# Performance work log

Hardware: AMD Instinct MI355X
Metric: run time of the kernel (lower is better)

The kernel has to match this reference:

```python
import jax, jax.numpy as jnp
import numpy as np

NEG = -1e30  # log-domain "zero" (safe in fp32/bf16 logaddexp)
EPS = 1e-7   # keras backend epsilon used by K.ctc_batch_cost


def setup_inputs() -> dict:
    key = jax.random.key(0)
    k1, k2 = jax.random.split(key)
    B, T, C, L = 64, 1024, 512, 128
    y_pred = jax.random.uniform(k1, (B, T, C), dtype=jnp.float32)
    y_true = jax.random.randint(k2, (B, L), 0, C - 1)  # blank = C-1 excluded
    return {"y_true": y_true, "y_pred": y_pred}


def ctc_batch_cost(y_true, y_pred):
    """Faithful jax port of keras.backend.ctc_batch_cost with full-length
    labels/inputs (as the CTCLayer passes input_length=T, label_length=L
    for every batch element). Returns per-example loss of shape [B, 1].

    K.ctc_batch_cost computes log(y_pred + eps) and feeds it to
    tf.nn.ctc_loss, which applies an internal softmax; we replicate that
    with log_softmax(log(y_pred + eps)). blank index = C - 1.
    """
    B, T, C = y_pred.shape
    L = y_true.shape[1]
    blank = C - 1
    logp = jax.nn.log_softmax(jnp.log(y_pred + EPS), axis=-1)  # [B,T,C]

    # Extended label sequence with interleaved blanks: length S = 2L+1
    S = 2 * L + 1
    ext = jnp.full((B, S), blank, dtype=y_true.dtype).at[:, 1::2].set(y_true)
    ext_m2 = jnp.concatenate(
        [jnp.full((B, 2), -1, dtype=ext.dtype), ext[:, :-2]], axis=1)
    # alpha[s-2] -> alpha[s] skip allowed iff ext[s] != blank and ext[s] != ext[s-2]
    skip = (ext != blank) & (ext != ext_m2)  # [B,S]

    # Emission log-probs gathered along the extended sequence: [B,T,S]
    emit = jnp.take_along_axis(
        logp, jnp.broadcast_to(ext[:, None, :], (B, T, S)), axis=2)

    # alpha_0: only states 0 (blank) and 1 (first label) are reachable
    alpha0 = (jnp.full((B, S), NEG, dtype=logp.dtype)
              .at[:, 0].set(emit[:, 0, 0])
              .at[:, 1].set(emit[:, 0, 1]))

    neg1 = jnp.full((B, 1), NEG, dtype=logp.dtype)
    neg2 = jnp.full((B, 2), NEG, dtype=logp.dtype)

    def step(alpha, emit_t):
        a1 = jnp.concatenate([neg1, alpha[:, :-1]], axis=1)   # stay->next
        a2 = jnp.concatenate([neg2, alpha[:, :-2]], axis=1)   # skip blank
        a2 = jnp.where(skip, a2, NEG)
        comb = jnp.logaddexp(jnp.logaddexp(alpha, a1), a2)
        return comb + emit_t, None

    emit_tm = jnp.transpose(emit, (1, 0, 2))  # time-major [T,B,S]
    alphaT, _ = jax.lax.scan(step, alpha0, emit_tm[1:])

    # p(labels) = alpha_T[S-1] + alpha_T[S-2]
    loss = -jnp.logaddexp(alphaT[:, -1], alphaT[:, -2])  # [B]
    return loss[:, None]


def reference(y_true, y_pred):
    return ctc_batch_cost(y_true, y_pred)
```

## Files before the change

kernel.cpp:

```cpp
#include <hip/hip_runtime.h>


#define EPSF 1e-7f
static constexpr int NB = 64;
static constexpr int NT = 1024;
static constexpr int NC = 512;
static constexpr int NL = 128;
static constexpr int CHUNK = 32;
static constexpr int NCH = NT / CHUNK;

typedef unsigned int uint32;
typedef float v2f __attribute__((ext_vector_type(2)));

__device__ __forceinline__ unsigned short rn_bf16(float x) {
    uint32 b = __float_as_uint(x);
    return (unsigned short)((b + 0x7FFFu + ((b >> 16) & 1u)) >> 16);
}

__global__ __launch_bounds__(256) void ctc_prep(const float* __restrict__ Y,
                                                const int* __restrict__ y_true,
                                                uint32* __restrict__ qlab,
                                                float* __restrict__ eblank,
                                                int mode) {
    const int lane = threadIdx.x & 63;
    const int wslot = threadIdx.x >> 6;
    const int nw = gridDim.x * 4;

    for (int w = blockIdx.x * 4 + wslot; w < NB * NT; w += nw) {
        int b = w >> 10;
        const float* row = Y + (size_t)w * NC;

        float4 v0 = *reinterpret_cast<const float4*>(row + lane * 4);
        float4 v1 = *reinterpret_cast<const float4*>(row + (NC / 2) + lane * 4);
        float s = ((v0.x + v0.y) + (v0.z + v0.w)) +
                  ((v1.x + v1.y) + (v1.z + v1.w));
#pragma unroll
        for (int d = 1; d < 64; d <<= 1) s += __shfl_xor(s, d);

        if (mode == 1) {
            float rb = row[NC - 1] + EPSF;
            float inv = 1.0f / (s + NC * EPSF);
            float rbi = 1.0f / rb;
            int2 lp = *reinterpret_cast<const int2*>(y_true + b * NL + lane * 2);
            float qx = (row[lp.x] + EPSF) * rbi;
            float qy = (row[lp.y] + EPSF) * rbi;
            uint32 pk = (uint32)rn_bf16(qx) | ((uint32)rn_bf16(qy) << 16);
            qlab[(size_t)w * (NL / 2) + lane] = pk;
            if (lane == 0) eblank[w] = rb * inv;
        } else {
            if (lane == 0) eblank[w] = 256.0f / (s + NC * EPSF);
        }
    }
}

__device__ __forceinline__ float dpp_wave_shr1(float x) {
    return __int_as_float(__builtin_amdgcn_update_dpp(
        0, __float_as_int(x), 0x138, 0xF, 0xF, true));
}

__device__ __forceinline__ float dpp_wave_max(float m) {
#define DPPMAX_(ctrl)                                                     \
    m = fmaxf(m, __int_as_float(__builtin_amdgcn_update_dpp(              \
                     0, __float_as_int(m), ctrl, 0xF, 0xF, true)))
    DPPMAX_(0x111); DPPMAX_(0x112); DPPMAX_(0x114); DPPMAX_(0x118);
    DPPMAX_(0x142); DPPMAX_(0x143);
#undef DPPMAX_
    return __int_as_float(
        __builtin_amdgcn_readlane(__float_as_int(m), 63));
}

__device__ __forceinline__ float dpp_wave_sum63(float v) {
#define DPPADD_(ctrl)                                                     \
    v += __int_as_float(__builtin_amdgcn_update_dpp(                      \
        0, __float_as_int(v), ctrl, 0xF, 0xF, true))
    DPPADD_(0x111); DPPADD_(0x112); DPPADD_(0x114); DPPADD_(0x118);
    DPPADD_(0x142); DPPADD_(0x143);
#undef DPPADD_
    return v;
}

__global__ __launch_bounds__(64) void ctc_rec1(const uint32* __restrict__ A,
                                               const float* __restrict__ Bv,
                                               const int* __restrict__ y_true,
                                               float* __restrict__ out) {
    const int b = blockIdx.x;
    const int l = threadIdx.x;
    const int* lab = y_true + b * NL;

    int lab_m1 = (l == 0) ? -1 : lab[2 * l - 1];
    int lab0 = lab[2 * l];
    int lab1 = lab[2 * l + 1];
    v2f SK = {(lab0 != lab_m1) ? 1.0f : 0.0f,
              (lab1 != lab0) ? 1.0f : 0.0f};

    float slog = 0.0f;
#pragma unroll
    for (int k = 0; k < NT / 64; k++)
        slog += logf(Bv[b * NT + k * 64 + l]);
    float sred = dpp_wave_sum63(slog);

    v2f X = {(l == 0) ? 1.0f : 0.0f, 0.0f};
    v2f Y = {0.0f, 0.0f};
    float pS = 0.0f;
    int ksum = 0;

    uint32 La[CHUNK], Lb[CHUNK];

    auto load = [&](int c, uint32(&L)[CHUNK]) {
        const uint32* base = A + ((size_t)b * NT + c * CHUNK) * (NL / 2) + l;
#pragma unroll
        for (int j = 0; j < CHUNK; j++) L[j] = base[(size_t)j * (NL / 2)];
    };

    auto process = [&](uint32(&L)[CHUNK]) {
#pragma unroll
        for (int j = 0; j < CHUNK; j++) {
            float s3 = dpp_wave_shr1(Y.y);
            v2f Q = {__uint_as_float(L[j] << 16),
                     __uint_as_float(L[j] & 0xFFFF0000u)};
            v2f S = {s3, Y.x};
            v2f T = X + Y;
            pS += Y.y;
            v2f nY = (T + SK * S) * Q;
            X = X + S;
            Y = nY;
        }
        v2f M2 = {fmaxf(X.x, Y.x), fmaxf(X.y, Y.y)};
        float m = fmaxf(M2.x, M2.y);
        m = fmaxf(m, (l == 63) ? pS : 0.0f);
        float mall = fmaxf(dpp_wave_max(m), 1e-30f);
        int e = (int)(__float_as_uint(mall) >> 23) - 127;
        float sc = __uint_as_float((uint32)(127 - e) << 23);
        X = X * sc; Y = Y * sc; pS *= sc;
        ksum += e;
    };

    load(0, La);
    for (int c = 0; c < NCH; c += 2) {
        __builtin_amdgcn_sched_barrier(0);
        if (c + 1 < NCH) load(c + 1, Lb);
        __builtin_amdgcn_sched_barrier(0);
        process(La);
        __builtin_amdgcn_sched_barrier(0);
        if (c + 2 < NCH) load(c + 2, La);
        __builtin_amdgcn_sched_barrier(0);
        process(Lb);
    }

    if (l == 63) {
        float tot = Y.y + pS;
        out[b] = -(logf(tot) + (float)ksum * 0.69314718055994531f + sred);
    }
}

__global__ __launch_bounds__(64) void ctc_rec0(const float* __restrict__ A,
                                               const float* __restrict__ Bv,
                                               const int* __restrict__ y_true,
                                               float* __restrict__ out) {
    const int b = blockIdx.x;
    const int l = threadIdx.x;
    const int* lab = y_true + b * NL;

    int lab_m1 = (l == 0) ? -1 : lab[2 * l - 1];
    int lab0 = lab[2 * l];
    int lab1 = lab[2 * l + 1];
    float sk0 = (lab0 != lab_m1) ? 1.0f : 0.0f;
    float sk1 = (lab1 != lab0) ? 1.0f : 0.0f;

    float p0 = (l == 0) ? 1.0f : 0.0f;
    float p1 = 0.0f, p2 = 0.0f, p3 = 0.0f, pS = 0.0f;
    int ksum = 0;

    for (int t = 0; t < NT; t++) {
        const float* base = A + ((size_t)b * NT + t) * NC;
        float iv = Bv[b * NT + t];
        float eb = (base[NC - 1] + EPSF) * iv;
        float ex = (base[lab0] + EPSF) * iv;
        float ey = (base[lab1] + EPSF) * iv;
        float s3 = dpp_wave_shr1(p3);
        float n0 = (p0 + s3) * eb;
        float n1 = (p1 + p0 + sk0 * s3) * ex;
        float n2 = (p2 + p1) * eb;
        float n3 = (p3 + p2 + sk1 * p1) * ey;
        pS = (pS + p3) * eb;
        p0 = n0; p1 = n1; p2 = n2; p3 = n3;
        if ((t & 15) == 15) {
            float m = fmaxf(fmaxf(p0, p1), fmaxf(p2, p3));
            m = fmaxf(m, (l == 63) ? pS : 0.0f);
            float mall = fmaxf(dpp_wave_max(m), 1e-30f);
            int e = (int)(__float_as_uint(mall) >> 23) - 127;
            float sc = __uint_as_float((uint32)(127 - e) << 23);
            p0 *= sc; p1 *= sc; p2 *= sc; p3 *= sc; pS *= sc;
            ksum += e;
        }
    }

    if (l == 63) {
        float tot = p3 + pS;
        out[b] = -(logf(tot) +
                   (float)(ksum - 8192) * 0.69314718055994531f);
    }
}

extern "C" void kernel_launch(void* const* d_in, const int* in_sizes, int n_in,
                              void* d_out, int out_size, void* d_ws, size_t ws_size,
                              hipStream_t stream) {
    const int* y_true = (const int*)d_in[0];
    const float* y_pred = (const float*)d_in[1];
    float* out = (float*)d_out;

    const size_t qlab_bytes = (size_t)NB * NT * (NL / 2) * sizeof(uint32);
    const size_t eb_bytes = (size_t)NB * NT * sizeof(float);

    if (ws_size >= qlab_bytes + eb_bytes) {
        uint32* qlab = (uint32*)d_ws;
        float* eblank = (float*)((char*)d_ws + qlab_bytes);
        ctc_prep<<<2048, 256, 0, stream>>>(y_pred, y_true, qlab, eblank, 1);
        ctc_rec1<<<NB, 64, 0, stream>>>(qlab, eblank, y_true, out);
    } else {
        float* invb = (float*)d_ws;
        ctc_prep<<<2048, 256, 0, stream>>>(y_pred, y_true, nullptr, invb, 0);
        ctc_rec0<<<NB, 64, 0, stream>>>(y_pred, invb, y_true, out);
    }
}
```

Baseline: 56.14 us.

## Interleave two batch recurrences per wavefront in CTC alpha kernel

Each wavefront of the recurrence kernel now advances two batch elements at once, interleaving their independent dependency chains to hide DPP and ALU latency. The grid is halved to 32 blocks and the chunk size drops from 32 to 16 to keep the doubled register buffers affordable. The cost is half as many waves across the GPU's CUs, so less parallelism, plus more register pressure and more frequent rescale reductions.

```diff
diff --git a/kernel.cpp b/kernel.cpp
--- a/kernel.cpp
+++ b/kernel.cpp
@@ -6,7 +6,7 @@
 static constexpr int NT = 1024;
 static constexpr int NC = 512;
 static constexpr int NL = 128;
-static constexpr int CHUNK = 32;
+static constexpr int CHUNK = 16;
 static constexpr int NCH = NT / CHUNK;
 
 typedef unsigned int uint32;
@@ -83,73 +83,102 @@
                                                const float* __restrict__ Bv,
                                                const int* __restrict__ y_true,
                                                float* __restrict__ out) {
-    const int b = blockIdx.x;
+    const int ba = blockIdx.x * 2;
+    const int bb = ba + 1;
     const int l = threadIdx.x;
-    const int* lab = y_true + b * NL;
-
-    int lab_m1 = (l == 0) ? -1 : lab[2 * l - 1];
-    int lab0 = lab[2 * l];
-    int lab1 = lab[2 * l + 1];
-    v2f SK = {(lab0 != lab_m1) ? 1.0f : 0.0f,
-              (lab1 != lab0) ? 1.0f : 0.0f};
-
-    float slog = 0.0f;
-#pragma unroll
-    for (int k = 0; k < NT / 64; k++)
-        slog += logf(Bv[b * NT + k * 64 + l]);
-    float sred = dpp_wave_sum63(slog);
-
-    v2f X = {(l == 0) ? 1.0f : 0.0f, 0.0f};
-    v2f Y = {0.0f, 0.0f};
-    float pS = 0.0f;
-    int ksum = 0;
-
-    uint32 La[CHUNK], Lb[CHUNK];
-
-    auto load = [&](int c, uint32(&L)[CHUNK]) {
-        const uint32* base = A + ((size_t)b * NT + c * CHUNK) * (NL / 2) + l;
-#pragma unroll
-        for (int j = 0; j < CHUNK; j++) L[j] = base[(size_t)j * (NL / 2)];
+
+    const int* labA = y_true + ba * NL;
+    const int* labB = y_true + bb * NL;
+    int am1 = (l == 0) ? -1 : labA[2 * l - 1];
+    int a0 = labA[2 * l];
+    int a1 = labA[2 * l + 1];
+    int bm1 = (l == 0) ? -1 : labB[2 * l - 1];
+    int b0 = labB[2 * l];
+    int b1 = labB[2 * l + 1];
+    v2f SKa = {(a0 != am1) ? 1.0f : 0.0f, (a1 != a0) ? 1.0f : 0.0f};
+    v2f SKb = {(b0 != bm1) ? 1.0f : 0.0f, (b1 != b0) ? 1.0f : 0.0f};
+
+    float slogA = 0.0f, slogB = 0.0f;
+#pragma unroll
+    for (int k = 0; k < NT / 64; k++) {
+        slogA += logf(Bv[ba * NT + k * 64 + l]);
+        slogB += logf(Bv[bb * NT + k * 64 + l]);
+    }
+    float sredA = dpp_wave_sum63(slogA);
+    float sredB = dpp_wave_sum63(slogB);
+
+    v2f Xa = {(l == 0) ? 1.0f : 0.0f, 0.0f}, Ya = {0.0f, 0.0f};
+    v2f Xb = {(l == 0) ? 1.0f : 0.0f, 0.0f}, Yb = {0.0f, 0.0f};
+    float pSa = 0.0f, pSb = 0.0f;
+    int ksA = 0, ksB = 0;
+
+    uint32 LA0[CHUNK], LB0[CHUNK], LA1[CHUNK], LB1[CHUNK];
+
+    auto load = [&](int c, uint32(&LA)[CHUNK], uint32(&LB)[CHUNK]) {
+        const uint32* pa = A + ((size_t)ba * NT + c * CHUNK) * (NL / 2) + l;
+        const uint32* pb = A + ((size_t)bb * NT + c * CHUNK) * (NL / 2) + l;
+#pragma unroll
+        for (int j = 0; j < CHUNK; j++) {
+            LA[j] = pa[(size_t)j * (NL / 2)];
+            LB[j] = pb[(size_t)j * (NL / 2)];
+        }
     };
 
-    auto process = [&](uint32(&L)[CHUNK]) {
+    auto process = [&](uint32(&LA)[CHUNK], uint32(&LB)[CHUNK]) {
 #pragma unroll
         for (int j = 0; j < CHUNK; j++) {
-            float s3 = dpp_wave_shr1(Y.y);
-            v2f Q = {__uint_as_float(L[j] << 16),
-                     __uint_as_float(L[j] & 0xFFFF0000u)};
-            v2f S = {s3, Y.x};
-            v2f T = X + Y;
-            pS += Y.y;
-            v2f nY = (T + SK * S) * Q;
-            X = X + S;
-            Y = nY;
-        }
-        v2f M2 = {fmaxf(X.x, Y.x), fmaxf(X.y, Y.y)};
-        float m = fmaxf(M2.x, M2.y);
-        m = fmaxf(m, (l == 63) ? pS : 0.0f);
-        float mall = fmaxf(dpp_wave_max(m), 1e-30f);
-        int e = (int)(__float_as_uint(mall) >> 23) - 127;
-        float sc = __uint_as_float((uint32)(127 - e) << 23);
-        X = X * sc; Y = Y * sc; pS *= sc;
-        ksum += e;
+            float s3a = dpp_wave_shr1(Ya.y);
+            float s3b = dpp_wave_shr1(Yb.y);
+            v2f Qa = {__uint_as_float(LA[j] << 16),
+                      __uint_as_float(LA[j] & 0xFFFF0000u)};
+            v2f Qb = {__uint_as_float(LB[j] << 16),
+                      __uint_as_float(LB[j] & 0xFFFF0000u)};
+            v2f Sa = {s3a, Ya.x};
+            v2f Sb = {s3b, Yb.x};
+            v2f Ta = Xa + Ya;
+            v2f Tb = Xb + Yb;
+            pSa += Ya.y;
+            pSb += Yb.y;
+            v2f nYa = (Ta + SKa * Sa) * Qa;
+            v2f nYb = (Tb + SKb * Sb) * Qb;
+            Xa = Xa + Sa;
+            Xb = Xb + Sb;
+            Ya = nYa;
+            Yb = nYb;
+        }
+        float ma = fmaxf(fmaxf(Xa.x, Ya.x), fmaxf(Xa.y, Ya.y));
+        float mb = fmaxf(fmaxf(Xb.x, Yb.x), fmaxf(Xb.y, Yb.y));
+        ma = fmaxf(ma, (l == 63) ? pSa : 0.0f);
+        mb = fmaxf(mb, (l == 63) ? pSb : 0.0f);
+        float mallA = fmaxf(dpp_wave_max(ma), 1e-30f);
+        float mallB = fmaxf(dpp_wave_max(mb), 1e-30f);
+        int ea = (int)(__float_as_uint(mallA) >> 23) - 127;
+        int eb = (int)(__float_as_uint(mallB) >> 23) - 127;
+        float sca = __uint_as_float((uint32)(127 - ea) << 23);
+        float scb = __uint_as_float((uint32)(127 - eb) << 23);
+        Xa = Xa * sca; Ya = Ya * sca; pSa *= sca;
+        Xb = Xb * scb; Yb = Yb * scb; pSb *= scb;
+        ksA += ea;
+        ksB += eb;
     };
 
-    load(0, La);
+    load(0, LA0, LB0);
     for (int c = 0; c < NCH; c += 2) {
         __builtin_amdgcn_sched_barrier(0);
-        if (c + 1 < NCH) load(c + 1, Lb);
-        __builtin_amdgcn_sched_barrier(0);
-        process(La);
-        __builtin_amdgcn_sched_barrier(0);
-        if (c + 2 < NCH) load(c + 2, La);
-        __builtin_amdgcn_sched_barrier(0);
-        process(Lb);
+        if (c + 1 < NCH) load(c + 1, LA1, LB1);
+        __builtin_amdgcn_sched_barrier(0);
+        process(LA0, LB0);
+        __builtin_amdgcn_sched_barrier(0);
+        if (c + 2 < NCH) load(c + 2, LA0, LB0);
+        __builtin_amdgcn_sched_barrier(0);
+        process(LA1, LB1);
     }
 
     if (l == 63) {
-        float tot = Y.y + pS;
-        out[b] = -(logf(tot) + (float)ksum * 0.69314718055994531f + sred);
+        out[ba] = -(logf(Ya.y + pSa) +
+                    (float)ksA * 0.69314718055994531f + sredA);
+        out[bb] = -(logf(Yb.y + pSb) +
+                    (float)ksB * 0.69314718055994531f + sredB);
     }
 }
 
@@ -216,7 +245,7 @@
         uint32* qlab = (uint32*)d_ws;
         float* eblank = (float*)((char*)d_ws + qlab_bytes);
         ctc_prep<<<2048, 256, 0, stream>>>(y_pred, y_true, qlab, eblank, 1);
-        ctc_rec1<<<NB, 64, 0, stream>>>(qlab, eblank, y_true, out);
+        ctc_rec1<<<NB / 2, 64, 0, stream>>>(qlab, eblank, y_true, out);
     } else {
         float* invb = (float*)d_ws;
         ctc_prep<<<2048, 256, 0, stream>>>(y_pred, y_true, nullptr, invb, 0);
```

Measured after the change: 83.31 us. 48.4% more time.

## Fuse prep and recurrence into one producer-consumer kernel with chunk flags

Applied to the files above, without the earlier changes.

Merges the emission-prep kernel and the alpha recurrence into a single launch. Producer blocks write bf16 label ratios chunk by chunk, accumulate log-normaliser sums atomically and publish per-chunk release flags. Consumer waves for each batch spin on those flags, so the serial recurrence starts while the rest of the prep is still running instead of waiting for a whole separate kernel. This adds a flag-zeroing kernel, spin-wait and atomic overhead, and relies on consumer and producer blocks being resident at the same time to avoid deadlock. It also halves the chunk size.

```diff
diff --git a/kernel.cpp b/kernel.cpp
--- a/kernel.cpp
+++ b/kernel.cpp
@@ -2,12 +2,12 @@
 
 
 #define EPSF 1e-7f
-static constexpr int NB = 64;
-static constexpr int NT = 1024;
-static constexpr int NC = 512;
-static constexpr int NL = 128;
-static constexpr int CHUNK = 32;
-static constexpr int NCH = NT / CHUNK;
+static constexpr int NB = 64, NT = 1024, NC = 512, NL = 128;
+static constexpr int CH = 16;
+static constexpr int NCHK = NT / CH;
+static constexpr int KPB = 16;
+static constexpr int PRODB = NB * KPB;
+static constexpr int RND = NCHK / KPB;
 
 typedef unsigned int uint32;
 typedef float v2f __attribute__((ext_vector_type(2)));
@@ -17,43 +17,7 @@
     return (unsigned short)((b + 0x7FFFu + ((b >> 16) & 1u)) >> 16);
 }
 
-__global__ __launch_bounds__(256) void ctc_prep(const float* __restrict__ Y,
-                                                const int* __restrict__ y_true,
-                                                uint32* __restrict__ qlab,
-                                                float* __restrict__ eblank,
-                                                int mode) {
-    const int lane = threadIdx.x & 63;
-    const int wslot = threadIdx.x >> 6;
-    const int nw = gridDim.x * 4;
-
-    for (int w = blockIdx.x * 4 + wslot; w < NB * NT; w += nw) {
-        int b = w >> 10;
-        const float* row = Y + (size_t)w * NC;
-
-        float4 v0 = *reinterpret_cast<const float4*>(row + lane * 4);
-        float4 v1 = *reinterpret_cast<const float4*>(row + (NC / 2) + lane * 4);
-        float s = ((v0.x + v0.y) + (v0.z + v0.w)) +
-                  ((v1.x + v1.y) + (v1.z + v1.w));
-#pragma unroll
-        for (int d = 1; d < 64; d <<= 1) s += __shfl_xor(s, d);
-
-        if (mode == 1) {
-            float rb = row[NC - 1] + EPSF;
-            float inv = 1.0f / (s + NC * EPSF);
-            float rbi = 1.0f / rb;
-            int2 lp = *reinterpret_cast<const int2*>(y_true + b * NL + lane * 2);
-            float qx = (row[lp.x] + EPSF) * rbi;
-            float qy = (row[lp.y] + EPSF) * rbi;
-            uint32 pk = (uint32)rn_bf16(qx) | ((uint32)rn_bf16(qy) << 16);
-            qlab[(size_t)w * (NL / 2) + lane] = pk;
-            if (lane == 0) eblank[w] = rb * inv;
-        } else {
-            if (lane == 0) eblank[w] = 256.0f / (s + NC * EPSF);
-        }
-    }
-}
-
-__device__ __forceinline__ float dpp_wave_shr1(float x) {
+__device__ __forceinline__ float dpp_shr1(float x) {
     return __int_as_float(__builtin_amdgcn_update_dpp(
         0, __float_as_int(x), 0x138, 0xF, 0xF, true));
 }
@@ -69,64 +33,110 @@
         __builtin_amdgcn_readlane(__float_as_int(m), 63));
 }
 
-__device__ __forceinline__ float dpp_wave_sum63(float v) {
-#define DPPADD_(ctrl)                                                     \
-    v += __int_as_float(__builtin_amdgcn_update_dpp(                      \
-        0, __float_as_int(v), ctrl, 0xF, 0xF, true))
-    DPPADD_(0x111); DPPADD_(0x112); DPPADD_(0x114); DPPADD_(0x118);
-    DPPADD_(0x142); DPPADD_(0x143);
-#undef DPPADD_
-    return v;
-}
-
-__global__ __launch_bounds__(64) void ctc_rec1(const uint32* __restrict__ A,
-                                               const float* __restrict__ Bv,
-                                               const int* __restrict__ y_true,
-                                               float* __restrict__ out) {
-    const int b = blockIdx.x;
+__global__ void ctc_zero(uint32* __restrict__ f, int n) {
+    int i = blockIdx.x * 256 + threadIdx.x;
+    if (i < n) f[i] = 0u;
+}
+
+__global__ __launch_bounds__(256) void ctc_fused(
+    const float* __restrict__ Yp, const int* __restrict__ y_true,
+    uint32* __restrict__ qlab, uint32* __restrict__ flags,
+    float* __restrict__ sumlog, float* __restrict__ out) {
+    __shared__ float sl[4];
+    const int bid = blockIdx.x;
+
+    if (bid >= NB) {
+        const int p = bid - NB;
+        const int b = p & (NB - 1);
+        const int k = p >> 6;
+        const int lane = threadIdx.x & 63;
+        const int wslot = threadIdx.x >> 6;
+        int2 lp = *reinterpret_cast<const int2*>(y_true + b * NL + lane * 2);
+
+        for (int r = 0; r < RND; ++r) {
+            int c = k + r * KPB;
+            float wlog = 0.0f;
+#pragma unroll
+            for (int i = 0; i < 4; ++i) {
+                int w = b * NT + c * CH + wslot * 4 + i;
+                const float* row = Yp + (size_t)w * NC;
+                float4 v0 = *reinterpret_cast<const float4*>(row + lane * 4);
+                float4 v1 =
+                    *reinterpret_cast<const float4*>(row + NC / 2 + lane * 4);
+                float s = ((v0.x + v0.y) + (v0.z + v0.w)) +
+                          ((v1.x + v1.y) + (v1.z + v1.w));
+#pragma unroll
+                for (int d = 1; d < 64; d <<= 1) s += __shfl_xor(s, d);
+                float rb = row[NC - 1] + EPSF;
+                float rbi = 1.0f / rb;
+                float qx = (row[lp.x] + EPSF) * rbi;
+                float qy = (row[lp.y] + EPSF) * rbi;
+                qlab[(size_t)w * (NL / 2) + lane] =
+                    (uint32)rn_bf16(qx) | ((uint32)rn_bf16(qy) << 16);
+                wlog += logf(rb * (1.0f / (s + NC * EPSF)));
+            }
+            if (lane == 0) sl[wslot] = wlog;
+            __syncthreads();
+            if (threadIdx.x == 0) {
+                atomicAdd(sumlog + b, sl[0] + sl[1] + sl[2] + sl[3]);
+                __hip_atomic_store(flags + b * NCHK + c, 1u, __ATOMIC_RELEASE,
+                                   __HIP_MEMORY_SCOPE_AGENT);
+            }
+            __syncthreads();
+        }
+        return;
+    }
+
+    if (threadIdx.x >= 64) return;
+    const int b = bid;
     const int l = threadIdx.x;
     const int* lab = y_true + b * NL;
 
     int lab_m1 = (l == 0) ? -1 : lab[2 * l - 1];
     int lab0 = lab[2 * l];
     int lab1 = lab[2 * l + 1];
-    v2f SK = {(lab0 != lab_m1) ? 1.0f : 0.0f,
-              (lab1 != lab0) ? 1.0f : 0.0f};
-
-    float slog = 0.0f;
-#pragma unroll
-    for (int k = 0; k < NT / 64; k++)
-        slog += logf(Bv[b * NT + k * 64 + l]);
-    float sred = dpp_wave_sum63(slog);
+    v2f SK = {(lab0 != lab_m1) ? 1.0f : 0.0f, (lab1 != lab0) ? 1.0f : 0.0f};
 
     v2f X = {(l == 0) ? 1.0f : 0.0f, 0.0f};
     v2f Y = {0.0f, 0.0f};
     float pS = 0.0f;
     int ksum = 0;
 
-    uint32 La[CHUNK], Lb[CHUNK];
-
-    auto load = [&](int c, uint32(&L)[CHUNK]) {
-        const uint32* base = A + ((size_t)b * NT + c * CHUNK) * (NL / 2) + l;
-#pragma unroll
-        for (int j = 0; j < CHUNK; j++) L[j] = base[(size_t)j * (NL / 2)];
-    };
-
-    auto process = [&](uint32(&L)[CHUNK]) {
-#pragma unroll
-        for (int j = 0; j < CHUNK; j++) {
-            float s3 = dpp_wave_shr1(Y.y);
-            v2f Q = {__uint_as_float(L[j] << 16),
-                     __uint_as_float(L[j] & 0xFFFF0000u)};
+    const uint32* fb = flags + b * NCHK;
+    const uint32* qb = qlab + (size_t)b * NT * (NL / 2) + l;
+    uint32 La[CH], Lb[CH];
+
+    auto peek = [&](int c) -> uint32 {
+        return __hip_atomic_load(fb + c, __ATOMIC_RELAXED,
+                                 __HIP_MEMORY_SCOPE_AGENT);
+    };
+    auto waitf = [&](int c) {
+        while (__hip_atomic_load(fb + c, __ATOMIC_ACQUIRE,
+                                 __HIP_MEMORY_SCOPE_AGENT) == 0u)
+            __builtin_amdgcn_s_sleep(2);
+    };
+    auto loadq = [&](int c, uint32(&L)[CH]) {
+        const uint32* base = qb + (size_t)c * CH * (NL / 2);
+#pragma unroll
+        for (int j = 0; j < CH; ++j)
+            L[j] = __hip_atomic_load(base + (size_t)j * (NL / 2),
+                                     __ATOMIC_RELAXED,
+                                     __HIP_MEMORY_SCOPE_AGENT);
+    };
+    auto process = [&](uint32(&L)[CH]) {
+#pragma unroll
+        for (int j = 0; j < CH; ++j) {
+            float s3 = dpp_shr1(Y.y);
+            v2f Qv = {__uint_as_float(L[j] << 16),
+                      __uint_as_float(L[j] & 0xFFFF0000u)};
             v2f S = {s3, Y.x};
             v2f T = X + Y;
             pS += Y.y;
-            v2f nY = (T + SK * S) * Q;
+            v2f nY = (T + SK * S) * Qv;
             X = X + S;
             Y = nY;
         }
-        v2f M2 = {fmaxf(X.x, Y.x), fmaxf(X.y, Y.y)};
-        float m = fmaxf(M2.x, M2.y);
+        float m = fmaxf(fmaxf(X.x, Y.x), fmaxf(X.y, Y.y));
         m = fmaxf(m, (l == 63) ? pS : 0.0f);
         float mall = fmaxf(dpp_wave_max(m), 1e-30f);
         int e = (int)(__float_as_uint(mall) >> 23) - 127;
@@ -135,21 +145,48 @@
         ksum += e;
     };
 
-    load(0, La);
-    for (int c = 0; c < NCH; c += 2) {
-        __builtin_amdgcn_sched_barrier(0);
-        if (c + 1 < NCH) load(c + 1, Lb);
+    waitf(0);
+    waitf(1);
+    loadq(0, La);
+    for (int c = 0; c < NCHK; c += 2) {
+        uint32 f2 = (c + 2 < NCHK) ? peek(c + 2) : 1u;
+        loadq(c + 1, Lb);
         __builtin_amdgcn_sched_barrier(0);
         process(La);
         __builtin_amdgcn_sched_barrier(0);
-        if (c + 2 < NCH) load(c + 2, La);
+        if (f2 == 0u) waitf(c + 2);
+        __builtin_amdgcn_sched_barrier(0);
+        uint32 f3 = (c + 3 < NCHK) ? peek(c + 3) : 1u;
+        if (c + 2 < NCHK) loadq(c + 2, La);
         __builtin_amdgcn_sched_barrier(0);
         process(Lb);
+        __builtin_amdgcn_sched_barrier(0);
+        if (f3 == 0u) waitf(c + 3);
+        __builtin_amdgcn_sched_barrier(0);
     }
 
     if (l == 63) {
+        float sred = __hip_atomic_load(sumlog + b, __ATOMIC_ACQUIRE,
+                                       __HIP_MEMORY_SCOPE_AGENT);
         float tot = Y.y + pS;
         out[b] = -(logf(tot) + (float)ksum * 0.69314718055994531f + sred);
+    }
+}
+
+__global__ __launch_bounds__(256) void ctc_prep0(const float* __restrict__ Y,
+                                                 float* __restrict__ invb) {
+    const int lane = threadIdx.x & 63;
+    const int wslot = threadIdx.x >> 6;
+    const int nw = gridDim.x * 4;
+    for (int w = blockIdx.x * 4 + wslot; w < NB * NT; w += nw) {
+        const float* row = Y + (size_t)w * NC;
+        float4 v0 = *reinterpret_cast<const float4*>(row + lane * 4);
+        float4 v1 = *reinterpret_cast<const float4*>(row + NC / 2 + lane * 4);
+        float s = ((v0.x + v0.y) + (v0.z + v0.w)) +
+                  ((v1.x + v1.y) + (v1.z + v1.w));
+#pragma unroll
+        for (int d = 1; d < 64; d <<= 1) s += __shfl_xor(s, d);
+        if (lane == 0) invb[w] = 256.0f / (s + NC * EPSF);
     }
 }
 
@@ -177,7 +214,7 @@
         float eb = (base[NC - 1] + EPSF) * iv;
         float ex = (base[lab0] + EPSF) * iv;
         float ey = (base[lab1] + EPSF) * iv;
-        float s3 = dpp_wave_shr1(p3);
+        float s3 = dpp_shr1(p3);
         float n0 = (p0 + s3) * eb;
         float n1 = (p1 + p0 + sk0 * s3) * ex;
         float n2 = (p2 + p1) * eb;
@@ -197,8 +234,7 @@
 
     if (l == 63) {
         float tot = p3 + pS;
-        out[b] = -(logf(tot) +
-                   (float)(ksum - 8192) * 0.69314718055994531f);
+        out[b] = -(logf(tot) + (float)(ksum - 8192) * 0.69314718055994531f);
     }
 }
 
@@ -210,16 +246,20 @@
     float* out = (float*)d_out;
 
     const size_t qlab_bytes = (size_t)NB * NT * (NL / 2) * sizeof(uint32);
-    const size_t eb_bytes = (size_t)NB * NT * sizeof(float);
-
-    if (ws_size >= qlab_bytes + eb_bytes) {
+    const int nflag = NB * NCHK;
+    const int nzero = nflag + NB;
+    const size_t need = qlab_bytes + (size_t)nzero * 4;
+
+    if (ws_size >= need) {
         uint32* qlab = (uint32*)d_ws;
-        float* eblank = (float*)((char*)d_ws + qlab_bytes);
-        ctc_prep<<<2048, 256, 0, stream>>>(y_pred, y_true, qlab, eblank, 1);
-        ctc_rec1<<<NB, 64, 0, stream>>>(qlab, eblank, y_true, out);
+        uint32* flags = (uint32*)((char*)d_ws + qlab_bytes);
+        float* sumlog = (float*)(flags + nflag);
+        ctc_zero<<<(nzero + 255) / 256, 256, 0, stream>>>(flags, nzero);
+        ctc_fused<<<NB + PRODB, 256, 0, stream>>>(y_pred, y_true, qlab, flags,
+                                                  sumlog, out);
     } else {
         float* invb = (float*)d_ws;
-        ctc_prep<<<2048, 256, 0, stream>>>(y_pred, y_true, nullptr, invb, 0);
+        ctc_prep0<<<2048, 256, 0, stream>>>(y_pred, invb);
         ctc_rec0<<<NB, 64, 0, stream>>>(y_pred, invb, y_true, out);
     }
 }
```

Measured after the change: 180.7 us. +221.9%, slower.
